# Optimization experiments

Measured on AMD Instinct MI355X. Metric: run time of the kernel, lower is better.

Reference implementation:

```python
import jax, jax.numpy as jnp
import numpy as np

EPS = 1e-12  # torch F.normalize eps

def _l2norm(t, axis):
    n = jnp.linalg.norm(t, axis=axis, keepdims=True)
    return t / jnp.maximum(n, EPS)

def setup_inputs() -> dict:
    key = jax.random.key(0)
    ks = jax.random.split(key, 7)
    B, L, D, F, K = 16, 128, 512, 1024, 16
    return {
        "x": jax.random.normal(ks[0], (B, L, D), jnp.float32),
        "W_gate_basis": jax.random.normal(ks[1], (K, D, F), jnp.float32) * (1.0 / np.sqrt(D)),
        "W_up_basis": jax.random.normal(ks[2], (K, D, F), jnp.float32) * (1.0 / np.sqrt(D)),
        "W_down_basis": jax.random.normal(ks[3], (K, F, D), jnp.float32) * (1.0 / np.sqrt(F)),
        "token_coef1": jax.random.normal(ks[4], (L, K), jnp.float32),
        "token_coef2": jax.random.normal(ks[5], (L, K), jnp.float32),
        "token_coef3": jax.random.normal(ks[6], (L, K), jnp.float32),
        "u_scale_param": jnp.ones((1, F), jnp.float32),
        "v_scale_param": jnp.ones((1, F), jnp.float32),
    }

def reference(x, W_gate_basis, W_up_basis, W_down_basis,
              token_coef1, token_coef2, token_coef3,
              u_scale_param, v_scale_param):
    D = x.shape[-1]
    c1 = jax.nn.softmax(token_coef1, axis=-1)
    c2 = jax.nn.softmax(token_coef2, axis=-1)
    c3 = jax.nn.softmax(token_coef3, axis=-1)
    # per-token weights [L, D, F] / [L, F, D]
    W_gate = jnp.einsum('lk,kio->lio', c1, W_gate_basis)
    W_up = jnp.einsum('lk,kio->lio', c2, W_up_basis)
    W_down = jnp.einsum('lk,koj->loj', c3, W_down_basis)
    W_gate = _l2norm(W_gate, axis=1)   # normalize over input dim D
    W_up = _l2norm(W_up, axis=1)
    W_down = _l2norm(W_down, axis=1)   # normalize over hidden dim F
    u = jnp.einsum('bld,ldf->blf', x, W_gate)
    v = jnp.einsum('bld,ldf->blf', x, W_up)
    u_scale = jnp.abs(u_scale_param) * 1.0
    v_scale = jnp.abs(v_scale_param) * jnp.sqrt(jnp.float32(D))
    h = jax.nn.silu(v_scale * v) * (u_scale * u)
    out = jnp.einsum('blf,lfd->bld', h, W_down)
    return _l2norm(out, axis=-1)
```

## Files before the change

### kernel.cpp

```cpp
#include <hip/hip_runtime.h>
#include <hip/hip_bf16.h>
#include <cmath>


typedef _Float16 half8 __attribute__((ext_vector_type(8)));
typedef _Float16 half4 __attribute__((ext_vector_type(4)));
typedef float    f32x4 __attribute__((ext_vector_type(4)));

#define MFMA_F16 __builtin_amdgcn_mfma_f32_16x16x32_f16

static constexpr size_t OFF_P1 = 0;
static constexpr size_t OFF_P2 = 16777216;
static constexpr size_t OFF_P3 = 33554432;
static constexpr size_t OFF_HP = 50331648;
static constexpr size_t WS_FAST = OFF_HP + 4194304;

__global__ __launch_bounds__(256) void prep_basis_all(
    const float* __restrict__ wg, const float* __restrict__ wu,
    const float* __restrict__ wd,
    _Float16* __restrict__ P1, _Float16* __restrict__ P2,
    _Float16* __restrict__ P3, int zoff)
{
    int z = blockIdx.y + zoff;
    const float* src = (z == 0) ? wg : (z == 1) ? wu : wd;
    _Float16*    dst = (z == 0) ? P1 : (z == 1) ? P2 : P3;
    int Amin = (z == 2) ? 1024 : 512;
    int Bmaj = (z == 2) ? 512 : 1024;
    int nM = Bmaj >> 4;
    int m0 = (blockIdx.x / nM) * 32;
    int M0 = (blockIdx.x % nM) * 16;

    __shared__ float S[16 * 544];
    int t = threadIdx.x;

    int row = (t >> 2) & 31;
    int cg  = t & 3;
    int khi = t >> 7;
#pragma unroll
    for (int p = 0; p < 8; ++p) {
        int k = p * 2 + khi;
        f32x4 v = *(const f32x4*)(
            src + (size_t)k * Amin * Bmaj + (size_t)(m0 + row) * Bmaj + M0 + cg * 4);
#pragma unroll
        for (int j = 0; j < 4; ++j)
            S[k * 544 + row * 17 + cg * 4 + j] = v[j];
    }
    __syncthreads();

    int mn = t & 31, mjb = t >> 5;
#pragma unroll
    for (int q = 0; q < 2; ++q) {
        int mj = mjb + q * 8;
        half8 v0, v1;
#pragma unroll
        for (int k = 0; k < 8; ++k) v0[k] = (_Float16)S[k * 544 + mn * 17 + mj];
#pragma unroll
        for (int k = 0; k < 8; ++k) v1[k] = (_Float16)S[(k + 8) * 544 + mn * 17 + mj];
        _Float16* out = dst + ((size_t)(M0 + mj) * Amin + m0 + mn) * 16;
        *(half8*)out       = v0;
        *(half8*)(out + 8) = v1;
    }
}

__global__ __launch_bounds__(256) void prep_x(
    const float* __restrict__ x, _Float16* __restrict__ XA)
{
    int l = blockIdx.x >> 1, bh = blockIdx.x & 1;
    __shared__ __align__(16) _Float16 XT[8][524];
    int t = threadIdx.x;

    int bl = t >> 5, q = t & 31;
    int b = bh * 8 + bl;
#pragma unroll
    for (int j = 0; j < 4; ++j) {
        f32x4 v = *(const f32x4*)(x + ((size_t)(b * 128 + l) * 512 + j * 128 + q * 4));
#pragma unroll
        for (int i = 0; i < 4; ++i)
            XT[bl][j * 128 + q * 4 + i] = (_Float16)v[i];
    }
    __syncthreads();

    int c = t >> 2, bi = t & 3;
#pragma unroll
    for (int s = 0; s < 2; ++s) {
        int blw = bi * 2 + s;
        half8 h = *(const half8*)(&XT[blw][c * 8]);
        *(half8*)(XA + (((size_t)(l * 64 + c) * 16 + bh * 8 + blw) * 8)) = h;
    }
}

__global__ __launch_bounds__(256, 2) void up_fast(
    const _Float16* __restrict__ P1, const _Float16* __restrict__ P2,
    const _Float16* __restrict__ XA,
    const float* __restrict__ tc1, const float* __restrict__ tc2,
    const float* __restrict__ usp, const float* __restrict__ vsp,
    _Float16* __restrict__ Hp)
{
    int lg = blockIdx.x >> 6;
    int f0 = (blockIdx.x & 63) * 16;
    int tid = threadIdx.x;
    int w = tid >> 6, lane = tid & 63;
    int n = lane & 15, kc = lane >> 4;
    bool ld = (kc < 2);

    __shared__ __align__(16) _Float16 Wt[2][2][16 * 584];
    __shared__ float CN[2 * 256];

    const _Float16* pP1 = P1 + ((size_t)(f0 + w * 4) * 512 + n) * 16 + kc * 8;
    const _Float16* pP2 = P2 + ((size_t)(f0 + w * 4) * 512 + n) * 16 + kc * 8;
    const _Float16* pXA = XA + (((size_t)(lg * 16 + w * 4) * 64 + kc) * 16 + n) * 8;

    half8 pa0[4][2], pa1[4][2];
#pragma unroll
    for (int fl = 0; fl < 4; ++fl)
#pragma unroll
        for (int dg = 0; dg < 2; ++dg) {
            half8 a = { 0, 0, 0, 0, 0, 0, 0, 0 };
            half8 b = { 0, 0, 0, 0, 0, 0, 0, 0 };
            if (ld) {
                a = *(const half8*)(pP1 + fl * 8192 + dg * 256);
                b = *(const half8*)(pP2 + fl * 8192 + dg * 256);
            }
            pa0[fl][dg] = a;
            pa1[fl][dg] = b;
        }
    const _Float16* qP1 = pP1 + 512;
    const _Float16* qP2 = pP2 + 512;

    if (tid < 32) {
        int s = tid >> 4, ll = tid & 15;
        const float* row = (s ? tc2 : tc1) + (size_t)(lg * 16 + ll) * 16;
        float e[16], m = -1e30f, sum = 0.f;
#pragma unroll
        for (int k = 0; k < 16; ++k) m = fmaxf(m, row[k]);
#pragma unroll
        for (int k = 0; k < 16; ++k) { e[k] = __expf(row[k] - m); sum += e[k]; }
        float r = 1.f / sum;
#pragma unroll
        for (int k = 0; k < 16; ++k) CN[s * 256 + ll * 16 + k] = e[k] * r;
    }
    __syncthreads();

    half8 cf1 = { 0, 0, 0, 0, 0, 0, 0, 0 };
    half8 cf2 = { 0, 0, 0, 0, 0, 0, 0, 0 };
    if (ld) {
#pragma unroll
        for (int j = 0; j < 8; ++j) {
            cf1[j] = (_Float16)CN[0 * 256 + n * 16 + kc * 8 + j];
            cf2[j] = (_Float16)CN[1 * 256 + n * 16 + kc * 8 + j];
        }
    }

    f32x4 zf = { 0.f, 0.f, 0.f, 0.f };
    f32x4 aU[4], aV[4];
#pragma unroll
    for (int i = 0; i < 4; ++i) { aU[i] = zf; aV[i] = zf; }
    float nsqU[4] = { 0.f, 0.f, 0.f, 0.f };
    float nsqV[4] = { 0.f, 0.f, 0.f, 0.f };
    half8 xf[4];

#pragma unroll 1
    for (int it = 0; it < 16; ++it) {
        _Float16* WtA = &Wt[it & 1][0][0];
        _Float16* WtB = &Wt[it & 1][1][0];
        const _Float16* RdA = &Wt[(it & 1) ^ 1][0][0];
        const _Float16* RdB = &Wt[(it & 1) ^ 1][1][0];

#pragma unroll
        for (int fl = 0; fl < 4; ++fl) {
            int f_l = w * 4 + fl;
#pragma unroll
            for (int dg = 0; dg < 2; ++dg) {
                f32x4 c1 = MFMA_F16(pa0[fl][dg], cf1, zf, 0, 0, 0);
                nsqU[fl] += c1[0] * c1[0] + c1[1] * c1[1]
                          + c1[2] * c1[2] + c1[3] * c1[3];
                half4 h1 = { (_Float16)c1[0], (_Float16)c1[1],
                             (_Float16)c1[2], (_Float16)c1[3] };
                *(half4*)(&WtA[n * 584 + f_l * 36 + dg * 16 + kc * 4]) = h1;
            }
        }
        if (it < 15) {
#pragma unroll
            for (int fl = 0; fl < 4; ++fl)
#pragma unroll
                for (int dg = 0; dg < 2; ++dg) {
                    half8 a = { 0, 0, 0, 0, 0, 0, 0, 0 };
                    if (ld) a = *(const half8*)(qP1 + fl * 8192 + dg * 256);
                    pa0[fl][dg] = a;
                }
        }
#pragma unroll
        for (int fl = 0; fl < 4; ++fl) {
            int f_l = w * 4 + fl;
#pragma unroll
            for (int dg = 0; dg < 2; ++dg) {
                f32x4 c2 = MFMA_F16(pa1[fl][dg], cf2, zf, 0, 0, 0);
                nsqV[fl] += c2[0] * c2[0] + c2[1] * c2[1]
                          + c2[2] * c2[2] + c2[3] * c2[3];
                half4 h2 = { (_Float16)c2[0], (_Float16)c2[1],
                             (_Float16)c2[2], (_Float16)c2[3] };
                *(half4*)(&WtB[n * 584 + f_l * 36 + dg * 16 + kc * 4]) = h2;
            }
        }
        if (it < 15) {
#pragma unroll
            for (int fl = 0; fl < 4; ++fl)
#pragma unroll
                for (int dg = 0; dg < 2; ++dg) {
                    half8 a = { 0, 0, 0, 0, 0, 0, 0, 0 };
                    if (ld) a = *(const half8*)(qP2 + fl * 8192 + dg * 256);
                    pa1[fl][dg] = a;
                }
        }
        if (it > 0) {
#pragma unroll
            for (int li = 0; li < 4; ++li) {
                int l = w * 4 + li;
                half8 wU = *(const half8*)(&RdA[l * 584 + n * 36 + kc * 8]);
                half8 wV = *(const half8*)(&RdB[l * 584 + n * 36 + kc * 8]);
                aU[li] = MFMA_F16(xf[li], wU, aU[li], 0, 0, 0);
                aV[li] = MFMA_F16(xf[li], wV, aV[li], 0, 0, 0);
            }
        }
#pragma unroll
        for (int li = 0; li < 4; ++li)
            xf[li] = *(const half8*)(pXA + li * 8192);
        pXA += 512;
        qP1 += 512;
        qP2 += 512;
        __syncthreads();
    }
#pragma unroll
    for (int li = 0; li < 4; ++li) {
        int l = w * 4 + li;
        half8 wU = *(const half8*)(&Wt[1][0][l * 584 + n * 36 + kc * 8]);
        half8 wV = *(const half8*)(&Wt[1][1][l * 584 + n * 36 + kc * 8]);
        aU[li] = MFMA_F16(xf[li], wU, aU[li], 0, 0, 0);
        aV[li] = MFMA_F16(xf[li], wV, aV[li], 0, 0, 0);
    }

#pragma unroll
    for (int fl = 0; fl < 4; ++fl) {
        float vU = nsqU[fl], vV = nsqV[fl];
        vU += __shfl_xor(vU, 16); vU += __shfl_xor(vU, 32);
        vV += __shfl_xor(vV, 16); vV += __shfl_xor(vV, 32);
        if (kc == 0) {
            CN[0 * 256 + n * 16 + w * 4 + fl] = vU;
            CN[1 * 256 + n * 16 + w * 4 + fl] = vV;
        }
    }
    __syncthreads();

    int f = f0 + n;
    float usv = fabsf(usp[f]);
    float vsv = fabsf(vsp[f]) * 22.627416997969522f;
#pragma unroll
    for (int li = 0; li < 4; ++li) {
        int lgl = lg * 16 + w * 4 + li;
        float r1 = 1.f / fmaxf(sqrtf(CN[0 * 256 + (w * 4 + li) * 16 + n]), 1e-12f);
        float r2 = 1.f / fmaxf(sqrtf(CN[1 * 256 + (w * 4 + li) * 16 + n]), 1e-12f);
#pragma unroll
        for (int i = 0; i < 4; ++i) {
            float u = aU[li][i] * r1;
            float v = aV[li][i] * r2;
            float zz = vsv * v;
            float sil = zz / (1.f + __expf(-zz));
            float h = sil * (usv * u);
            Hp[(((size_t)lgl * 128 + (f >> 3)) * 16 + kc * 4 + i) * 8 + (f & 7)] =
                (_Float16)h;
        }
    }
}

__global__ __launch_bounds__(256, 2) void down_fast(
    const _Float16* __restrict__ P3, const float* __restrict__ tc3,
    const _Float16* __restrict__ Hp,
    float* __restrict__ Rp, float* __restrict__ Np)
{
    int zh = blockIdx.x >> 8;
    int rem = blockIdx.x & 255;
    int lg = rem >> 5;
    int d0 = (rem & 31) * 16;
    int tid = threadIdx.x;
    int w = tid >> 6, lane = tid & 63;
    int n = lane & 15, kc = lane >> 4;
    bool ld = (kc < 2);

    __shared__ __align__(16) _Float16 Wt[2][16 * 584];
    __shared__ float CN[256];

    const _Float16* pP3 = P3 + ((size_t)(d0 + w * 4) * 1024 + zh * 256 + n) * 16 + kc * 8;
    const _Float16* pHp = Hp + (((size_t)(lg * 16 + w * 4) * 128 + zh * 32 + kc) * 16 + n) * 8;

    half8 pa[4][2];
#pragma unroll
    for (int dl = 0; dl < 4; ++dl)
#pragma unroll
        for (int fg = 0; fg < 2; ++fg) {
            half8 a = { 0, 0, 0, 0, 0, 0, 0, 0 };
            if (ld) a = *(const half8*)(pP3 + dl * 16384 + fg * 256);
            pa[dl][fg] = a;
        }
    const _Float16* qP3 = pP3 + 512;

    if (tid < 16) {
        const float* row = tc3 + (size_t)(lg * 16 + tid) * 16;
        float e[16], m = -1e30f, sum = 0.f;
#pragma unroll
        for (int k = 0; k < 16; ++k) m = fmaxf(m, row[k]);
#pragma unroll
        for (int k = 0; k < 16; ++k) { e[k] = __expf(row[k] - m); sum += e[k]; }
        float r = 1.f / sum;
#pragma unroll
        for (int k = 0; k < 16; ++k) CN[tid * 16 + k] = e[k] * r;
    }
    __syncthreads();

    half8 cf3 = { 0, 0, 0, 0, 0, 0, 0, 0 };
    if (ld) {
#pragma unroll
        for (int j = 0; j < 8; ++j)
            cf3[j] = (_Float16)CN[n * 16 + kc * 8 + j];
    }

    f32x4 zf = { 0.f, 0.f, 0.f, 0.f };
    f32x4 aO[4];
#pragma unroll
    for (int i = 0; i < 4; ++i) aO[i] = zf;
    float nsqD[4] = { 0.f, 0.f, 0.f, 0.f };
    half8 hf[4];

#pragma unroll 1
    for (int it = 0; it < 8; ++it) {
        _Float16* WtW = &Wt[it & 1][0];
        const _Float16* WtR = &Wt[(it & 1) ^ 1][0];

#pragma unroll
        for (int dl = 0; dl < 4; ++dl) {
            int d_l = w * 4 + dl;
#pragma unroll
            for (int fg = 0; fg < 2; ++fg) {
                f32x4 cw = MFMA_F16(pa[dl][fg], cf3, zf, 0, 0, 0);
                nsqD[dl] += cw[0] * cw[0] + cw[1] * cw[1]
                          + cw[2] * cw[2] + cw[3] * cw[3];
                half4 h4 = { (_Float16)cw[0], (_Float16)cw[1],
                             (_Float16)cw[2], (_Float16)cw[3] };
                *(half4*)(&WtW[n * 584 + d_l * 36 + fg * 16 + kc * 4]) = h4;
            }
        }
        if (it < 7) {
#pragma unroll
            for (int dl = 0; dl < 4; ++dl)
#pragma unroll
                for (int fg = 0; fg < 2; ++fg) {
                    half8 a = { 0, 0, 0, 0, 0, 0, 0, 0 };
                    if (ld) a = *(const half8*)(qP3 + dl * 16384 + fg * 256);
                    pa[dl][fg] = a;
                }
        }
        if (it > 0) {
#pragma unroll
            for (int li = 0; li < 4; ++li) {
                int l = w * 4 + li;
                half8 wf = *(const half8*)(&WtR[l * 584 + n * 36 + kc * 8]);
                aO[li] = MFMA_F16(hf[li], wf, aO[li], 0, 0, 0);
            }
        }
#pragma unroll
        for (int li = 0; li < 4; ++li)
            hf[li] = *(const half8*)(pHp + li * 16384);
        pHp += 512;
        qP3 += 512;
        __syncthreads();
    }
#pragma unroll
    for (int li = 0; li < 4; ++li) {
        int l = w * 4 + li;
        half8 wf = *(const half8*)(&Wt[1][l * 584 + n * 36 + kc * 8]);
        aO[li] = MFMA_F16(hf[li], wf, aO[li], 0, 0, 0);
    }

#pragma unroll
    for (int dl = 0; dl < 4; ++dl) {
        float v = nsqD[dl];
        v += __shfl_xor(v, 16); v += __shfl_xor(v, 32);
        if (kc == 0)
            Np[(size_t)zh * 65536 + (size_t)(lg * 16 + n) * 512 + d0 + w * 4 + dl] = v;
    }
#pragma unroll
    for (int li = 0; li < 4; ++li) {
        int lgl = lg * 16 + w * 4 + li;
#pragma unroll
        for (int i = 0; i < 4; ++i)
            Rp[(size_t)zh * 1048576 +
               ((size_t)(kc * 4 + i) * 128 + lgl) * 512 + d0 + n] = aO[li][i];
    }
}

__global__ __launch_bounds__(128) void final_combine(
    const float* __restrict__ Rp, const float* __restrict__ Np,
    float* __restrict__ out)
{
    int rid = blockIdx.x;
    int l = rid & 127;
    int t = threadIdx.x;
    f32x4 r = { 0.f, 0.f, 0.f, 0.f };
    f32x4 nn = { 0.f, 0.f, 0.f, 0.f };
#pragma unroll
    for (int zh = 0; zh < 4; ++zh) {
        f32x4 rz = *(const f32x4*)(Rp + (size_t)zh * 1048576 + (size_t)rid * 512 + t * 4);
        f32x4 nz = *(const f32x4*)(Np + (size_t)zh * 65536 + (size_t)l * 512 + t * 4);
#pragma unroll
        for (int j = 0; j < 4; ++j) { r[j] += rz[j]; nn[j] += nz[j]; }
    }
    f32x4 y;
#pragma unroll
    for (int j = 0; j < 4; ++j) {
        float rr = 1.f / fmaxf(sqrtf(fmaxf(nn[j], 0.f)), 1e-12f);
        y[j] = r[j] * rr;
    }
    float s = y[0] * y[0] + y[1] * y[1] + y[2] * y[2] + y[3] * y[3];
#pragma unroll
    for (int off = 32; off > 0; off >>= 1) s += __shfl_down(s, off);
    __shared__ float sred[2];
    if ((t & 63) == 0) sred[t >> 6] = s;
    __syncthreads();
    float rr = 1.f / fmaxf(sqrtf(sred[0] + sred[1]), 1e-12f);
    f32x4 o = { y[0] * rr, y[1] * rr, y[2] * rr, y[3] * rr };
    *(f32x4*)(out + (size_t)rid * 512 + t * 4) = o;
}

__global__ __launch_bounds__(256) void up_kernel(
    const float* __restrict__ x,
    const float* __restrict__ wg, const float* __restrict__ wu,
    const float* __restrict__ tc1, const float* __restrict__ tc2,
    const float* __restrict__ usp, const float* __restrict__ vsp,
    _Float16* __restrict__ Hp)
{
    int lg = blockIdx.x >> 6;
    int f0 = (blockIdx.x & 63) * 16;
    int tid = threadIdx.x;
    int w = tid >> 6, lane = tid & 63;
    int n = lane & 15, kc = lane >> 4;

    __shared__ __align__(16) _Float16 Xt[256 * 40];
    __shared__ __align__(16) _Float16 Bh[32 * 16 * 24];
    __shared__ __align__(16) _Float16 Wt[16 * 528];
    __shared__ float CN[2 * 16 * 16];

    if (tid < 32) {
        int s = tid >> 4, ll = tid & 15;
        const float* row = (s ? tc2 : tc1) + (size_t)(lg * 16 + ll) * 16;
        float e[16], m = -1e30f, sum = 0.f;
#pragma unroll
        for (int k = 0; k < 16; ++k) m = fmaxf(m, row[k]);
#pragma unroll
        for (int k = 0; k < 16; ++k) { e[k] = __expf(row[k] - m); sum += e[k]; }
        float r = 1.f / sum;
#pragma unroll
        for (int k = 0; k < 16; ++k) CN[s * 256 + ll * 16 + k] = e[k] * r;
    }
    __syncthreads();

    half8 cf1 = { 0, 0, 0, 0, 0, 0, 0, 0 };
    half8 cf2 = { 0, 0, 0, 0, 0, 0, 0, 0 };
    if (kc < 2) {
#pragma unroll
        for (int j = 0; j < 8; ++j) {
            cf1[j] = (_Float16)CN[0 * 256 + n * 16 + kc * 8 + j];
            cf2[j] = (_Float16)CN[1 * 256 + n * 16 + kc * 8 + j];
        }
    }

    f32x4 zf = { 0.f, 0.f, 0.f, 0.f };
    f32x4 aU[4], aV[4];
#pragma unroll
    for (int i = 0; i < 4; ++i) { aU[i] = zf; aV[i] = zf; }
    float nsqU[4] = { 0.f, 0.f, 0.f, 0.f };
    float nsqV[4] = { 0.f, 0.f, 0.f, 0.f };

    for (int it = 0; it < 16; ++it) {
        int d0 = it * 32;
#pragma unroll
        for (int p = 0; p < 8; ++p) {
            int r = p * 32 + (tid >> 3);
            int fj = tid & 7;
            int ll = r >> 4, b = r & 15;
            f32x4 v = *(const f32x4*)(
                x + ((size_t)(b * 128 + lg * 16 + ll) * 512 + d0 + fj * 4));
            half4 h = { (_Float16)v[0], (_Float16)v[1],
                        (_Float16)v[2], (_Float16)v[3] };
            *(half4*)(&Xt[r * 40 + fj * 4]) = h;
        }
#pragma unroll
        for (int p = 0; p < 8; ++p) {
            int idx = p * 256 + tid;
            int q = idx & 3, dd = (idx >> 2) & 31, k = idx >> 7;
            f32x4 v = *(const f32x4*)(
                wg + ((size_t)k * 512 + d0 + dd) * 1024 + f0 + q * 4);
#pragma unroll
            for (int j = 0; j < 4; ++j)
                Bh[(dd * 16 + q * 4 + j) * 24 + k] = (_Float16)v[j];
        }
        __syncthreads();
#pragma unroll
        for (int fl = 0; fl < 4; ++fl) {
            int f_l = w * 4 + fl;
#pragma unroll
            for (int dg = 0; dg < 2; ++dg) {
                half8 a = { 0, 0, 0, 0, 0, 0, 0, 0 };
                if (kc < 2)
                    a = *(const half8*)(&Bh[((dg * 16 + n) * 16 + f_l) * 24 + kc * 8]);
                f32x4 cw = MFMA_F16(a, cf1, zf, 0, 0, 0);
                nsqU[fl] += cw[0] * cw[0] + cw[1] * cw[1]
                          + cw[2] * cw[2] + cw[3] * cw[3];
                half4 h4 = { (_Float16)cw[0], (_Float16)cw[1],
                             (_Float16)cw[2], (_Float16)cw[3] };
                *(half4*)(&Wt[n * 528 + f_l * 32 + dg * 16 + kc * 4]) = h4;
            }
        }
        __syncthreads();
#pragma unroll
        for (int li = 0; li < 4; ++li) {
            int l = w * 4 + li;
            half8 xf = *(const half8*)(&Xt[(l * 16 + n) * 40 + kc * 8]);
            half8 wf = *(const half8*)(&Wt[l * 528 + n * 32 + kc * 8]);
            aU[li] = MFMA_F16(xf, wf, aU[li], 0, 0, 0);
        }
#pragma unroll
        for (int p = 0; p < 8; ++p) {
            int idx = p * 256 + tid;
            int q = idx & 3, dd = (idx >> 2) & 31, k = idx >> 7;
            f32x4 v = *(const f32x4*)(
                wu + ((size_t)k * 512 + d0 + dd) * 1024 + f0 + q * 4);
#pragma unroll
            for (int j = 0; j < 4; ++j)
                Bh[(dd * 16 + q * 4 + j) * 24 + k] = (_Float16)v[j];
        }
        __syncthreads();
#pragma unroll
        for (int fl = 0; fl < 4; ++fl) {
            int f_l = w * 4 + fl;
#pragma unroll
            for (int dg = 0; dg < 2; ++dg) {
                half8 a = { 0, 0, 0, 0, 0, 0, 0, 0 };
                if (kc < 2)
                    a = *(const half8*)(&Bh[((dg * 16 + n) * 16 + f_l) * 24 + kc * 8]);
                f32x4 cw = MFMA_F16(a, cf2, zf, 0, 0, 0);
                nsqV[fl] += cw[0] * cw[0] + cw[1] * cw[1]
                          + cw[2] * cw[2] + cw[3] * cw[3];
                half4 h4 = { (_Float16)cw[0], (_Float16)cw[1],
                             (_Float16)cw[2], (_Float16)cw[3] };
                *(half4*)(&Wt[n * 528 + f_l * 32 + dg * 16 + kc * 4]) = h4;
            }
        }
        __syncthreads();
#pragma unroll
        for (int li = 0; li < 4; ++li) {
            int l = w * 4 + li;
            half8 xf = *(const half8*)(&Xt[(l * 16 + n) * 40 + kc * 8]);
            half8 wf = *(const half8*)(&Wt[l * 528 + n * 32 + kc * 8]);
            aV[li] = MFMA_F16(xf, wf, aV[li], 0, 0, 0);
        }
        __syncthreads();
    }

#pragma unroll
    for (int fl = 0; fl < 4; ++fl) {
        float vU = nsqU[fl], vV = nsqV[fl];
        vU += __shfl_xor(vU, 16); vU += __shfl_xor(vU, 32);
        vV += __shfl_xor(vV, 16); vV += __shfl_xor(vV, 32);
        if (kc == 0) {
            CN[0 * 256 + n * 16 + w * 4 + fl] = vU;
            CN[1 * 256 + n * 16 + w * 4 + fl] = vV;
        }
    }
    __syncthreads();

    int f = f0 + n;
    float usv = fabsf(usp[f]);
    float vsv = fabsf(vsp[f]) * 22.627416997969522f;
#pragma unroll
    for (int li = 0; li < 4; ++li) {
        int lgl = lg * 16 + w * 4 + li;
        float r1 = 1.f / fmaxf(sqrtf(CN[0 * 256 + (w * 4 + li) * 16 + n]), 1e-12f);
        float r2 = 1.f / fmaxf(sqrtf(CN[1 * 256 + (w * 4 + li) * 16 + n]), 1e-12f);
#pragma unroll
        for (int i = 0; i < 4; ++i) {
            float u = aU[li][i] * r1;
            float v = aV[li][i] * r2;
            float zz = vsv * v;
            float sil = zz / (1.f + __expf(-zz));
            float h = sil * (usv * u);
            Hp[((size_t)lgl * 16 + kc * 4 + i) * 1024 + f] = (_Float16)h;
        }
    }
}

__global__ __launch_bounds__(256) void down_kernel(
    const float* __restrict__ wd, const float* __restrict__ tc3,
    const _Float16* __restrict__ Hp, float* __restrict__ out)
{
    int lg = blockIdx.x >> 5;
    int d0 = (blockIdx.x & 31) * 16;
    int tid = threadIdx.x;
    int w = tid >> 6, lane = tid & 63;
    int n = lane & 15, kc = lane >> 4;

    __shared__ __align__(16) _Float16 Ht[256 * 40];
    __shared__ __align__(16) _Float16 Bh[32 * 16 * 24];
    __shared__ __align__(16) _Float16 Wt[16 * 528];
    __shared__ float CN[16 * 16];

    if (tid < 16) {
        const float* row = tc3 + (size_t)(lg * 16 + tid) * 16;
        float e[16], m = -1e30f, sum = 0.f;
#pragma unroll
        for (int k = 0; k < 16; ++k) m = fmaxf(m, row[k]);
#pragma unroll
        for (int k = 0; k < 16; ++k) { e[k] = __expf(row[k] - m); sum += e[k]; }
        float r = 1.f / sum;
#pragma unroll
        for (int k = 0; k < 16; ++k) CN[tid * 16 + k] = e[k] * r;
    }
    __syncthreads();

    half8 cf3 = { 0, 0, 0, 0, 0, 0, 0, 0 };
    if (kc < 2) {
#pragma unroll
        for (int j = 0; j < 8; ++j)
            cf3[j] = (_Float16)CN[n * 16 + kc * 8 + j];
    }

    f32x4 zf = { 0.f, 0.f, 0.f, 0.f };
    f32x4 aO[4];
#pragma unroll
    for (int i = 0; i < 4; ++i) aO[i] = zf;
    float nsqD[4] = { 0.f, 0.f, 0.f, 0.f };

    for (int it = 0; it < 32; ++it) {
        int f0 = it * 32;
#pragma unroll
        for (int p = 0; p < 8; ++p) {
            int r = p * 32 + (tid >> 3);
            int hj = tid & 7;
            int ll = r >> 4, b = r & 15;
            half4 v = *(const half4*)(
                Hp + ((size_t)(lg * 16 + ll) * 16 + b) * 1024 + f0 + hj * 4);
            *(half4*)(&Ht[r * 40 + hj * 4]) = v;
        }
#pragma unroll
        for (int p = 0; p < 8; ++p) {
            int idx = p * 256 + tid;
            int q = idx & 3, ff = (idx >> 2) & 31, k = idx >> 7;
            f32x4 v = *(const f32x4*)(
                wd + ((size_t)k * 1024 + f0 + ff) * 512 + d0 + q * 4);
#pragma unroll
            for (int j = 0; j < 4; ++j)
                Bh[(ff * 16 + q * 4 + j) * 24 + k] = (_Float16)v[j];
        }
        __syncthreads();
#pragma unroll
        for (int dl = 0; dl < 4; ++dl) {
            int d_l = w * 4 + dl;
#pragma unroll
            for (int fg = 0; fg < 2; ++fg) {
                half8 a = { 0, 0, 0, 0, 0, 0, 0, 0 };
                if (kc < 2)
                    a = *(const half8*)(&Bh[((fg * 16 + n) * 16 + d_l) * 24 + kc * 8]);
                f32x4 cw = MFMA_F16(a, cf3, zf, 0, 0, 0);
                nsqD[dl] += cw[0] * cw[0] + cw[1] * cw[1]
                          + cw[2] * cw[2] + cw[3] * cw[3];
                half4 h4 = { (_Float16)cw[0], (_Float16)cw[1],
                             (_Float16)cw[2], (_Float16)cw[3] };
                *(half4*)(&Wt[n * 528 + d_l * 32 + fg * 16 + kc * 4]) = h4;
            }
        }
        __syncthreads();
#pragma unroll
        for (int li = 0; li < 4; ++li) {
            int l = w * 4 + li;
            half8 hf = *(const half8*)(&Ht[(l * 16 + n) * 40 + kc * 8]);
            half8 wf = *(const half8*)(&Wt[l * 528 + n * 32 + kc * 8]);
            aO[li] = MFMA_F16(hf, wf, aO[li], 0, 0, 0);
        }
        __syncthreads();
    }

#pragma unroll
    for (int dl = 0; dl < 4; ++dl) {
        float v = nsqD[dl];
        v += __shfl_xor(v, 16); v += __shfl_xor(v, 32);
        if (kc == 0) CN[n * 16 + w * 4 + dl] = v;
    }
    __syncthreads();

#pragma unroll
    for (int li = 0; li < 4; ++li) {
        int lgl = lg * 16 + w * 4 + li;
        float r3 = 1.f / fmaxf(sqrtf(CN[(w * 4 + li) * 16 + n]), 1e-12f);
#pragma unroll
        for (int i = 0; i < 4; ++i)
            out[((size_t)(kc * 4 + i) * 128 + lgl) * 512 + d0 + n] = aO[li][i] * r3;
    }
}

__global__ __launch_bounds__(128) void final_kernel(float* __restrict__ out)
{
    int rid = blockIdx.x;
    int t = threadIdx.x;
    f32x4 y = *(const f32x4*)(out + (size_t)rid * 512 + t * 4);
    float s = y[0] * y[0] + y[1] * y[1] + y[2] * y[2] + y[3] * y[3];
#pragma unroll
    for (int off = 32; off > 0; off >>= 1) s += __shfl_down(s, off);
    __shared__ float sred[2];
    if ((t & 63) == 0) sred[t >> 6] = s;
    __syncthreads();
    float rr = 1.f / fmaxf(sqrtf(sred[0] + sred[1]), 1e-12f);
    f32x4 o = { y[0] * rr, y[1] * rr, y[2] * rr, y[3] * rr };
    *(f32x4*)(out + (size_t)rid * 512 + t * 4) = o;
}

extern "C" void kernel_launch(void* const* d_in, const int* in_sizes, int n_in,
                              void* d_out, int out_size, void* d_ws, size_t ws_size,
                              hipStream_t stream)
{
    (void)in_sizes; (void)n_in; (void)out_size;
    const float* x   = (const float*)d_in[0];
    const float* wg  = (const float*)d_in[1];
    const float* wu  = (const float*)d_in[2];
    const float* wd  = (const float*)d_in[3];
    const float* tc1 = (const float*)d_in[4];
    const float* tc2 = (const float*)d_in[5];
    const float* tc3 = (const float*)d_in[6];
    const float* usp = (const float*)d_in[7];
    const float* vsp = (const float*)d_in[8];
    float* outp = (float*)d_out;
    char* ws = (char*)d_ws;

    if (ws_size >= WS_FAST) {
        _Float16* P1 = (_Float16*)(ws + OFF_P1);
        _Float16* P2 = (_Float16*)(ws + OFF_P2);
        _Float16* P3 = (_Float16*)(ws + OFF_P3);
        _Float16* XA = (_Float16*)(ws + OFF_P3);
        _Float16* Hp = (_Float16*)(ws + OFF_HP);
        float* Rp = (float*)(ws + OFF_P1);
        float* Np = (float*)(ws + OFF_P2);
        prep_basis_all<<<dim3(1024, 2), dim3(256), 0, stream>>>(
            wg, wu, wd, P1, P2, P3, 0);
        prep_x<<<dim3(256), dim3(256), 0, stream>>>(x, XA);
        up_fast<<<dim3(512), dim3(256), 0, stream>>>(P1, P2, XA, tc1, tc2,
                                                     usp, vsp, Hp);
        prep_basis_all<<<dim3(1024, 1), dim3(256), 0, stream>>>(
            wg, wu, wd, P1, P2, P3, 2);
        down_fast<<<dim3(1024), dim3(256), 0, stream>>>(P3, tc3, Hp, Rp, Np);
        final_combine<<<dim3(2048), dim3(128), 0, stream>>>(Rp, Np, outp);
    } else {
        _Float16* Hp = (_Float16*)ws;
        up_kernel<<<dim3(512), dim3(256), 0, stream>>>(x, wg, wu, tc1, tc2,
                                                       usp, vsp, Hp);
        down_kernel<<<dim3(256), dim3(256), 0, stream>>>(wd, tc3, Hp, outp);
        final_kernel<<<dim3(2048), dim3(128), 0, stream>>>(outp);
    }
}
```

Before: 244.9 us.

## Split gate/up projection into separate blocks and fuse the product into the down kernel

The up kernel no longer computes both the gate and up projections in one block. Each block now handles one of them, which doubles the grid to 1024 blocks, halves LDS and register use, and raises the occupancy hint to 4. Each block writes either the scaled gate output or the silu(up) result to separate fp16 buffers. The down kernel loads both buffers and multiplies them in fp16 to form h. This adds an extra intermediate write and read, and computes the product in fp16 instead of fp32. The workspace is reshuffled so the down-basis buffer reuses memory that P2 and XA no longer need.

```diff
diff --git a/kernel.cpp b/kernel.cpp
--- a/kernel.cpp
+++ b/kernel.cpp
@@ -9,11 +9,13 @@
 
 #define MFMA_F16 __builtin_amdgcn_mfma_f32_16x16x32_f16
 
-static constexpr size_t OFF_P1 = 0;
-static constexpr size_t OFF_P2 = 16777216;
-static constexpr size_t OFF_P3 = 33554432;
-static constexpr size_t OFF_HP = 50331648;
-static constexpr size_t WS_FAST = OFF_HP + 4194304;
+static constexpr size_t OFF_P1  = 0;
+static constexpr size_t OFF_P2  = 16777216;
+static constexpr size_t OFF_P3n = 17825792;
+static constexpr size_t OFF_XA  = 33554432;
+static constexpr size_t OFF_U2  = 35651584;
+static constexpr size_t OFF_S   = 39845888;
+static constexpr size_t WS_FAST = 54525952;
 
 __global__ __launch_bounds__(256) void prep_basis_all(
     const float* __restrict__ wg, const float* __restrict__ wu,
@@ -30,7 +32,7 @@
     int m0 = (blockIdx.x / nM) * 32;
     int M0 = (blockIdx.x % nM) * 16;
 
-    __shared__ float S[16 * 544];
+    __shared__ float Sh[16 * 544];
     int t = threadIdx.x;
 
     int row = (t >> 2) & 31;
@@ -43,7 +45,7 @@
             src + (size_t)k * Amin * Bmaj + (size_t)(m0 + row) * Bmaj + M0 + cg * 4);
 #pragma unroll
         for (int j = 0; j < 4; ++j)
-            S[k * 544 + row * 17 + cg * 4 + j] = v[j];
+            Sh[k * 544 + row * 17 + cg * 4 + j] = v[j];
     }
     __syncthreads();
 
@@ -53,9 +55,9 @@
         int mj = mjb + q * 8;
         half8 v0, v1;
 #pragma unroll
-        for (int k = 0; k < 8; ++k) v0[k] = (_Float16)S[k * 544 + mn * 17 + mj];
-#pragma unroll
-        for (int k = 0; k < 8; ++k) v1[k] = (_Float16)S[(k + 8) * 544 + mn * 17 + mj];
+        for (int k = 0; k < 8; ++k) v0[k] = (_Float16)Sh[k * 544 + mn * 17 + mj];
+#pragma unroll
+        for (int k = 0; k < 8; ++k) v1[k] = (_Float16)Sh[(k + 8) * 544 + mn * 17 + mj];
         _Float16* out = dst + ((size_t)(M0 + mj) * Amin + m0 + mn) * 16;
         *(half8*)out       = v0;
         *(half8*)(out + 8) = v1;
@@ -89,47 +91,44 @@
     }
 }
 
-__global__ __launch_bounds__(256, 2) void up_fast(
+__global__ __launch_bounds__(256, 4) void up_split(
     const _Float16* __restrict__ P1, const _Float16* __restrict__ P2,
     const _Float16* __restrict__ XA,
     const float* __restrict__ tc1, const float* __restrict__ tc2,
     const float* __restrict__ usp, const float* __restrict__ vsp,
-    _Float16* __restrict__ Hp)
-{
-    int lg = blockIdx.x >> 6;
-    int f0 = (blockIdx.x & 63) * 16;
+    _Float16* __restrict__ U2, _Float16* __restrict__ S)
+{
+    int bid = blockIdx.x;
+    int mh = bid >> 9;
+    int lg = (bid >> 6) & 7;
+    int f0 = (bid & 63) * 16;
     int tid = threadIdx.x;
     int w = tid >> 6, lane = tid & 63;
     int n = lane & 15, kc = lane >> 4;
-    bool ld = (kc < 2);
-
-    __shared__ __align__(16) _Float16 Wt[2][2][16 * 584];
-    __shared__ float CN[2 * 256];
-
-    const _Float16* pP1 = P1 + ((size_t)(f0 + w * 4) * 512 + n) * 16 + kc * 8;
-    const _Float16* pP2 = P2 + ((size_t)(f0 + w * 4) * 512 + n) * 16 + kc * 8;
+    bool ldp = (kc < 2);
+
+    const _Float16* P  = mh ? P2 : P1;
+    const float*    tc = mh ? tc2 : tc1;
+
+    __shared__ __align__(16) _Float16 Wt[2][16 * 584];
+    __shared__ float CN[256];
+
+    const _Float16* pP  = P + ((size_t)(f0 + w * 4) * 512 + n) * 16 + kc * 8;
     const _Float16* pXA = XA + (((size_t)(lg * 16 + w * 4) * 64 + kc) * 16 + n) * 8;
 
-    half8 pa0[4][2], pa1[4][2];
+    half8 pa[4][2];
 #pragma unroll
     for (int fl = 0; fl < 4; ++fl)
 #pragma unroll
         for (int dg = 0; dg < 2; ++dg) {
             half8 a = { 0, 0, 0, 0, 0, 0, 0, 0 };
-            half8 b = { 0, 0, 0, 0, 0, 0, 0, 0 };
-            if (ld) {
-                a = *(const half8*)(pP1 + fl * 8192 + dg * 256);
-                b = *(const half8*)(pP2 + fl * 8192 + dg * 256);
-            }
-            pa0[fl][dg] = a;
-            pa1[fl][dg] = b;
-        }
-    const _Float16* qP1 = pP1 + 512;
-    const _Float16* qP2 = pP2 + 512;
-
-    if (tid < 32) {
-        int s = tid >> 4, ll = tid & 15;
-        const float* row = (s ? tc2 : tc1) + (size_t)(lg * 16 + ll) * 16;
+            if (ldp) a = *(const half8*)(pP + fl * 8192 + dg * 256);
+            pa[fl][dg] = a;
+        }
+    const _Float16* qP = pP + 512;
+
+    if (tid < 16) {
+        const float* row = tc + (size_t)(lg * 16 + tid) * 16;
         float e[16], m = -1e30f, sum = 0.f;
 #pragma unroll
         for (int k = 0; k < 16; ++k) m = fmaxf(m, row[k]);
@@ -137,46 +136,40 @@
         for (int k = 0; k < 16; ++k) { e[k] = __expf(row[k] - m); sum += e[k]; }
         float r = 1.f / sum;
 #pragma unroll
-        for (int k = 0; k < 16; ++k) CN[s * 256 + ll * 16 + k] = e[k] * r;
-    }
-    __syncthreads();
-
-    half8 cf1 = { 0, 0, 0, 0, 0, 0, 0, 0 };
-    half8 cf2 = { 0, 0, 0, 0, 0, 0, 0, 0 };
-    if (ld) {
-#pragma unroll
-        for (int j = 0; j < 8; ++j) {
-            cf1[j] = (_Float16)CN[0 * 256 + n * 16 + kc * 8 + j];
-            cf2[j] = (_Float16)CN[1 * 256 + n * 16 + kc * 8 + j];
-        }
+        for (int k = 0; k < 16; ++k) CN[tid * 16 + k] = e[k] * r;
+    }
+    __syncthreads();
+
+    half8 cf = { 0, 0, 0, 0, 0, 0, 0, 0 };
+    if (ldp) {
+#pragma unroll
+        for (int j = 0; j < 8; ++j)
+            cf[j] = (_Float16)CN[n * 16 + kc * 8 + j];
     }
 
     f32x4 zf = { 0.f, 0.f, 0.f, 0.f };
-    f32x4 aU[4], aV[4];
-#pragma unroll
-    for (int i = 0; i < 4; ++i) { aU[i] = zf; aV[i] = zf; }
-    float nsqU[4] = { 0.f, 0.f, 0.f, 0.f };
-    float nsqV[4] = { 0.f, 0.f, 0.f, 0.f };
+    f32x4 aU[4];
+#pragma unroll
+    for (int i = 0; i < 4; ++i) aU[i] = zf;
+    float nsq[4] = { 0.f, 0.f, 0.f, 0.f };
     half8 xf[4];
 
 #pragma unroll 1
     for (int it = 0; it < 16; ++it) {
-        _Float16* WtA = &Wt[it & 1][0][0];
-        _Float16* WtB = &Wt[it & 1][1][0];
-        const _Float16* RdA = &Wt[(it & 1) ^ 1][0][0];
-        const _Float16* RdB = &Wt[(it & 1) ^ 1][1][0];
+        _Float16* WtW = &Wt[it & 1][0];
+        const _Float16* WtR = &Wt[(it & 1) ^ 1][0];
 
 #pragma unroll
         for (int fl = 0; fl < 4; ++fl) {
             int f_l = w * 4 + fl;
 #pragma unroll
             for (int dg = 0; dg < 2; ++dg) {
-                f32x4 c1 = MFMA_F16(pa0[fl][dg], cf1, zf, 0, 0, 0);
-                nsqU[fl] += c1[0] * c1[0] + c1[1] * c1[1]
-                          + c1[2] * c1[2] + c1[3] * c1[3];
+                f32x4 c1 = MFMA_F16(pa[fl][dg], cf, zf, 0, 0, 0);
+                nsq[fl] += c1[0] * c1[0] + c1[1] * c1[1]
+                         + c1[2] * c1[2] + c1[3] * c1[3];
                 half4 h1 = { (_Float16)c1[0], (_Float16)c1[1],
                              (_Float16)c1[2], (_Float16)c1[3] };
-                *(half4*)(&WtA[n * 584 + f_l * 36 + dg * 16 + kc * 4]) = h1;
+                *(half4*)(&WtW[n * 584 + f_l * 36 + dg * 16 + kc * 4]) = h1;
             }
         }
         if (it < 15) {
@@ -185,96 +178,61 @@
 #pragma unroll
                 for (int dg = 0; dg < 2; ++dg) {
                     half8 a = { 0, 0, 0, 0, 0, 0, 0, 0 };
-                    if (ld) a = *(const half8*)(qP1 + fl * 8192 + dg * 256);
-                    pa0[fl][dg] = a;
-                }
-        }
-#pragma unroll
-        for (int fl = 0; fl < 4; ++fl) {
-            int f_l = w * 4 + fl;
-#pragma unroll
-            for (int dg = 0; dg < 2; ++dg) {
-                f32x4 c2 = MFMA_F16(pa1[fl][dg], cf2, zf, 0, 0, 0);
-                nsqV[fl] += c2[0] * c2[0] + c2[1] * c2[1]
-                          + c2[2] * c2[2] + c2[3] * c2[3];
-                half4 h2 = { (_Float16)c2[0], (_Float16)c2[1],
-                             (_Float16)c2[2], (_Float16)c2[3] };
-                *(half4*)(&WtB[n * 584 + f_l * 36 + dg * 16 + kc * 4]) = h2;
-            }
-        }
-        if (it < 15) {
-#pragma unroll
-            for (int fl = 0; fl < 4; ++fl)
-#pragma unroll
-                for (int dg = 0; dg < 2; ++dg) {
-                    half8 a = { 0, 0, 0, 0, 0, 0, 0, 0 };
-                    if (ld) a = *(const half8*)(qP2 + fl * 8192 + dg * 256);
-                    pa1[fl][dg] = a;
+                    if (ldp) a = *(const half8*)(qP + fl * 8192 + dg * 256);
+                    pa[fl][dg] = a;
                 }
         }
         if (it > 0) {
 #pragma unroll
             for (int li = 0; li < 4; ++li) {
                 int l = w * 4 + li;
-                half8 wU = *(const half8*)(&RdA[l * 584 + n * 36 + kc * 8]);
-                half8 wV = *(const half8*)(&RdB[l * 584 + n * 36 + kc * 8]);
+                half8 wU = *(const half8*)(&WtR[l * 584 + n * 36 + kc * 8]);
                 aU[li] = MFMA_F16(xf[li], wU, aU[li], 0, 0, 0);
-                aV[li] = MFMA_F16(xf[li], wV, aV[li], 0, 0, 0);
             }
         }
 #pragma unroll
         for (int li = 0; li < 4; ++li)
             xf[li] = *(const half8*)(pXA + li * 8192);
         pXA += 512;
-        qP1 += 512;
-        qP2 += 512;
+        qP += 512;
         __syncthreads();
     }
 #pragma unroll
     for (int li = 0; li < 4; ++li) {
         int l = w * 4 + li;
-        half8 wU = *(const half8*)(&Wt[1][0][l * 584 + n * 36 + kc * 8]);
-        half8 wV = *(const half8*)(&Wt[1][1][l * 584 + n * 36 + kc * 8]);
+        half8 wU = *(const half8*)(&Wt[1][l * 584 + n * 36 + kc * 8]);
         aU[li] = MFMA_F16(xf[li], wU, aU[li], 0, 0, 0);
-        aV[li] = MFMA_F16(xf[li], wV, aV[li], 0, 0, 0);
     }
 
 #pragma unroll
     for (int fl = 0; fl < 4; ++fl) {
-        float vU = nsqU[fl], vV = nsqV[fl];
+        float vU = nsq[fl];
         vU += __shfl_xor(vU, 16); vU += __shfl_xor(vU, 32);
-        vV += __shfl_xor(vV, 16); vV += __shfl_xor(vV, 32);
-        if (kc == 0) {
-            CN[0 * 256 + n * 16 + w * 4 + fl] = vU;
-            CN[1 * 256 + n * 16 + w * 4 + fl] = vV;
-        }
+        if (kc == 0) CN[n * 16 + w * 4 + fl] = vU;
     }
     __syncthreads();
 
     int f = f0 + n;
-    float usv = fabsf(usp[f]);
-    float vsv = fabsf(vsp[f]) * 22.627416997969522f;
+    float sc = mh ? (fabsf(vsp[f]) * 22.627416997969522f)
+                  : fabsf(usp[f]);
+    _Float16* Out = mh ? S : U2;
 #pragma unroll
     for (int li = 0; li < 4; ++li) {
         int lgl = lg * 16 + w * 4 + li;
-        float r1 = 1.f / fmaxf(sqrtf(CN[0 * 256 + (w * 4 + li) * 16 + n]), 1e-12f);
-        float r2 = 1.f / fmaxf(sqrtf(CN[1 * 256 + (w * 4 + li) * 16 + n]), 1e-12f);
+        float r1 = 1.f / fmaxf(sqrtf(CN[(w * 4 + li) * 16 + n]), 1e-12f);
 #pragma unroll
         for (int i = 0; i < 4; ++i) {
-            float u = aU[li][i] * r1;
-            float v = aV[li][i] * r2;
-            float zz = vsv * v;
-            float sil = zz / (1.f + __expf(-zz));
-            float h = sil * (usv * u);
-            Hp[(((size_t)lgl * 128 + (f >> 3)) * 16 + kc * 4 + i) * 8 + (f & 7)] =
-                (_Float16)h;
+            float val = aU[li][i] * r1 * sc;
+            if (mh) val = val / (1.f + __expf(-val));
+            Out[(((size_t)lgl * 128 + (f >> 3)) * 16 + kc * 4 + i) * 8 + (f & 7)] =
+                (_Float16)val;
         }
     }
 }
 
 __global__ __launch_bounds__(256, 2) void down_fast(
     const _Float16* __restrict__ P3, const float* __restrict__ tc3,
-    const _Float16* __restrict__ Hp,
+    const _Float16* __restrict__ S, const _Float16* __restrict__ U2,
     float* __restrict__ Rp, float* __restrict__ Np)
 {
     int zh = blockIdx.x >> 8;
@@ -284,13 +242,15 @@
     int tid = threadIdx.x;
     int w = tid >> 6, lane = tid & 63;
     int n = lane & 15, kc = lane >> 4;
-    bool ld = (kc < 2);
+    bool ldp = (kc < 2);
 
     __shared__ __align__(16) _Float16 Wt[2][16 * 584];
     __shared__ float CN[256];
 
     const _Float16* pP3 = P3 + ((size_t)(d0 + w * 4) * 1024 + zh * 256 + n) * 16 + kc * 8;
-    const _Float16* pHp = Hp + (((size_t)(lg * 16 + w * 4) * 128 + zh * 32 + kc) * 16 + n) * 8;
+    size_t hoff = (((size_t)(lg * 16 + w * 4) * 128 + zh * 32 + kc) * 16 + n) * 8;
+    const _Float16* pS = S + hoff;
+    const _Float16* pU = U2 + hoff;
 
     half8 pa[4][2];
 #pragma unroll
@@ -298,7 +258,7 @@
 #pragma unroll
         for (int fg = 0; fg < 2; ++fg) {
             half8 a = { 0, 0, 0, 0, 0, 0, 0, 0 };
-            if (ld) a = *(const half8*)(pP3 + dl * 16384 + fg * 256);
+            if (ldp) a = *(const half8*)(pP3 + dl * 16384 + fg * 256);
             pa[dl][fg] = a;
         }
     const _Float16* qP3 = pP3 + 512;
@@ -317,7 +277,7 @@
     __syncthreads();
 
     half8 cf3 = { 0, 0, 0, 0, 0, 0, 0, 0 };
-    if (ld) {
+    if (ldp) {
 #pragma unroll
         for (int j = 0; j < 8; ++j)
             cf3[j] = (_Float16)CN[n * 16 + kc * 8 + j];
@@ -354,7 +314,7 @@
 #pragma unroll
                 for (int fg = 0; fg < 2; ++fg) {
                     half8 a = { 0, 0, 0, 0, 0, 0, 0, 0 };
-                    if (ld) a = *(const half8*)(qP3 + dl * 16384 + fg * 256);
+                    if (ldp) a = *(const half8*)(qP3 + dl * 16384 + fg * 256);
                     pa[dl][fg] = a;
                 }
         }
@@ -367,9 +327,13 @@
             }
         }
 #pragma unroll
-        for (int li = 0; li < 4; ++li)
-            hf[li] = *(const half8*)(pHp + li * 16384);
-        pHp += 512;
+        for (int li = 0; li < 4; ++li) {
+            half8 s8 = *(const half8*)(pS + li * 16384);
+            half8 u8 = *(const half8*)(pU + li * 16384);
+            hf[li] = s8 * u8;
+        }
+        pS += 512;
+        pU += 512;
         qP3 += 512;
         __syncthreads();
     }
@@ -739,21 +703,22 @@
     char* ws = (char*)d_ws;
 
     if (ws_size >= WS_FAST) {
-        _Float16* P1 = (_Float16*)(ws + OFF_P1);
-        _Float16* P2 = (_Float16*)(ws + OFF_P2);
-        _Float16* P3 = (_Float16*)(ws + OFF_P3);
-        _Float16* XA = (_Float16*)(ws + OFF_P3);
-        _Float16* Hp = (_Float16*)(ws + OFF_HP);
+        _Float16* P1  = (_Float16*)(ws + OFF_P1);
+        _Float16* P2  = (_Float16*)(ws + OFF_P2);
+        _Float16* P3n = (_Float16*)(ws + OFF_P3n);
+        _Float16* XA  = (_Float16*)(ws + OFF_XA);
+        _Float16* U2  = (_Float16*)(ws + OFF_U2);
+        _Float16* S   = (_Float16*)(ws + OFF_S);
         float* Rp = (float*)(ws + OFF_P1);
         float* Np = (float*)(ws + OFF_P2);
         prep_basis_all<<<dim3(1024, 2), dim3(256), 0, stream>>>(
-            wg, wu, wd, P1, P2, P3, 0);
+            wg, wu, wd, P1, P2, P3n, 0);
         prep_x<<<dim3(256), dim3(256), 0, stream>>>(x, XA);
-        up_fast<<<dim3(512), dim3(256), 0, stream>>>(P1, P2, XA, tc1, tc2,
-                                                     usp, vsp, Hp);
+        up_split<<<dim3(1024), dim3(256), 0, stream>>>(P1, P2, XA, tc1, tc2,
+                                                       usp, vsp, U2, S);
         prep_basis_all<<<dim3(1024, 1), dim3(256), 0, stream>>>(
-            wg, wu, wd, P1, P2, P3, 2);
-        down_fast<<<dim3(1024), dim3(256), 0, stream>>>(P3, tc3, Hp, Rp, Np);
+            wg, wu, wd, P1, P2, P3n, 2);
+        down_fast<<<dim3(1024), dim3(256), 0, stream>>>(P3n, tc3, S, U2, Rp, Np);
         final_combine<<<dim3(2048), dim3(128), 0, stream>>>(Rp, Np, outp);
     } else {
         _Float16* Hp = (_Float16*)ws;
```

Measured after the change: 251.0 us. 1.02x slower.
